# Optimization experiments

Measured on AMD Instinct MI355X. Metric: run time of the kernel, lower is better.

Reference implementation:

```python
import jax, jax.numpy as jnp
import numpy as np
from jax import lax

# ---- config (mirrors TrinityGuidance init kwargs) ----
GAMMA = 10.0        # LSE smoothing
M = 64              # RUDY grid size
THRESH = 1.0        # congestion threshold
SIGMA = 1.5         # gaussian smoothing sigma
K_SOFT = 2.0        # soft-bbox sigmoid sharpness
W_WL, W_CONG = 1.0, 0.5

B, V, P, NN, MP = 4, 20000, 400000, 50000, 32

# 4 rotation matrices (0/90/180/270 deg)
R_ALL = jnp.array([[[1, 0], [0, 1]],
                   [[0, -1], [1, 0]],
                   [[-1, 0], [0, -1]],
                   [[0, 1], [-1, 0]]], dtype=jnp.float32)


def _gauss_kernel(sigma):
    ksize = max(int(4 * sigma) | 1, 3)
    x = jnp.arange(ksize, dtype=jnp.float32) - ksize // 2
    g = jnp.exp(-x ** 2 / (2.0 * sigma ** 2))
    g2 = g[None, :] * g[:, None]
    return g2 / g2.sum()  # (k,k)


def setup_inputs() -> dict:
    key = jax.random.key(0)
    ks = jax.random.split(key, 7)
    positions = jax.random.uniform(ks[0], (B, V, 2), minval=-1.0, maxval=1.0)
    pin_to_macro = jax.random.randint(ks[1], (P,), 0, V)
    pin_offsets = jax.random.normal(ks[2], (P, 2)) * 0.01
    n2p = jax.random.randint(ks[3], (NN, MP), 0, P)
    # ragged nets: first cnt pins valid, rest padded with -1 (cnt in [2, MP])
    cnt = jax.random.randint(ks[4], (NN, 1), 2, MP + 1)
    net_to_pin = jnp.where(jnp.arange(MP)[None, :] < cnt, n2p, -1)
    rot_idx = jax.random.randint(ks[5], (B, V), 0, 4)
    rotation_onehot = jax.nn.one_hot(rot_idx, 4, dtype=jnp.float32)
    net_weights = jax.random.uniform(ks[6], (NN,), minval=0.5, maxval=1.5)
    return dict(positions=positions, net_to_pin=net_to_pin,
                pin_to_macro=pin_to_macro, pin_offsets=pin_offsets,
                rotation_onehot=rotation_onehot, net_weights=net_weights)


def _forward(positions, pin_offsets, rotation_onehot, net_weights,
             net_to_pin, pin_to_macro):
    # --- pin positions with rotated offsets ---
    macro_pos = positions[:, pin_to_macro, :]            # (B,P,2) gather
    macro_rot = rotation_onehot[:, pin_to_macro, :]      # (B,P,4)
    Rm = jnp.einsum('bpk,kij->bpij', macro_rot, R_ALL)   # (B,P,2,2)
    rotated = jnp.einsum('bpij,pj->bpi', Rm, pin_offsets)
    pin_pos = macro_pos + rotated                        # (B,P,2)

    valid = net_to_pin >= 0                              # (NN,MP)
    safe = jnp.maximum(net_to_pin, 0)
    net_pin_pos = pin_pos[:, safe, :]                    # (B,NN,MP,2)
    maskf = valid[None, :, :, None]
    masked_max = jnp.where(maskf, net_pin_pos, -1e9)
    masked_min = jnp.where(maskf, net_pin_pos, 1e9)

    # --- WA wirelength via masked double logsumexp per net ---
    gamma = jnp.float32(GAMMA)
    lse_max = jax.nn.logsumexp(gamma * masked_max, axis=2) / gamma   # (B,NN,2)
    lse_min = -jax.nn.logsumexp(-gamma * masked_min, axis=2) / gamma
    wl_per_net = (lse_max - lse_min).sum(-1)             # (B,NN)
    hpwl = (wl_per_net * net_weights[None, :]).sum(1)    # (B,)

    # --- RUDY congestion (separable soft-bbox, no (B,N,M,M) materialization) ---
    bbox_max = masked_max.max(axis=2)                    # (B,NN,2)
    bbox_min = masked_min.min(axis=2)
    bmax = (bbox_max + 1.0) * 0.5 * (M - 1)
    bmin = (bbox_min + 1.0) * 0.5 * (M - 1)
    x_min, y_min = bmin[..., 0:1], bmin[..., 1:2]        # (B,NN,1)
    x_max, y_max = bmax[..., 0:1], bmax[..., 1:2]
    g = jnp.arange(M, dtype=jnp.float32)[None, None, :]  # (1,1,M)
    in_x = jax.nn.sigmoid(K_SOFT * (g - x_min + 0.5)) * \
           jax.nn.sigmoid(K_SOFT * (x_max - g + 0.5))    # (B,NN,M)
    in_y = jax.nn.sigmoid(K_SOFT * (g - y_min + 0.5)) * \
           jax.nn.sigmoid(K_SOFT * (y_max - g + 0.5))    # (B,NN,M)
    bbox_size = jnp.maximum((x_max - x_min + 1.0) * (y_max - y_min + 1.0), 1.0)
    # rudy[b,i,j] = sum_n in_y[b,n,i] * in_x[b,n,j] / bbox_size[b,n]
    rudy = jnp.einsum('bni,bnj->bij', in_y / bbox_size, in_x)
    rudy = rudy[:, None, :, :]                           # (B,1,M,M)

    kernel = _gauss_kernel(SIGMA)                        # (k,k)
    pad = kernel.shape[-1] // 2
    rudy_smooth = lax.conv_general_dilated(
        rudy, kernel[None, None, :, :],
        window_strides=(1, 1), padding=[(pad, pad), (pad, pad)],
        dimension_numbers=('NCHW', 'OIHW', 'NCHW'))
    overflow = jax.nn.relu(rudy_smooth - THRESH)
    penalty = (overflow ** 2).sum(axis=(1, 2, 3))        # (B,)

    return W_WL * hpwl + W_CONG * penalty                # (B,)


def reference(positions, net_to_pin, pin_to_macro, pin_offsets,
              rotation_onehot, net_weights):
    return _forward(positions, pin_offsets, rotation_onehot, net_weights,
                    net_to_pin, pin_to_macro)
```

## Files before the change

### kernel.cpp

```cpp
#include <hip/hip_runtime.h>
#include <cstddef>

namespace {

constexpr int B = 4, V = 20000, P = 400000, NN = 50000, MP = 32;
constexpr float GAMMA = 10.0f, INV_GAMMA = 0.1f;
constexpr float KSOFT = 2.0f;
constexpr float THRESH = 1.0f;
constexpr float W_WL = 1.0f, W_CONG = 0.5f;
constexpr int BPB = 128;
constexpr int NET_GRID = BPB * B;
constexpr int GRPS = 7;
constexpr int NPW = GRPS * 16;
constexpr int A_SUBS = 196;
constexpr int A_GRID = A_SUBS * B;
constexpr int PREP_N = NN * MP;

typedef __attribute__((ext_vector_type(8)))  short bf16x8;
typedef __attribute__((ext_vector_type(16))) float f32x16;

__device__ __forceinline__ float fast_rcp(float x) { return __builtin_amdgcn_rcpf(x); }
__device__ __forceinline__ short f2bf(float f) {
    unsigned u = __float_as_uint(f);
    u += 0x7fffu + ((u >> 16) & 1u);
    return (short)(u >> 16);
}
template <int CTRL>
__device__ __forceinline__ float dpp_mov(float x, float id) {
    return __int_as_float(__builtin_amdgcn_update_dpp(
        __float_as_int(id), __float_as_int(x), CTRL, 0xf, 0xf, false));
}
__device__ __forceinline__ float rdlane(float x, int l) {
    return __int_as_float(__builtin_amdgcn_readlane(__float_as_int(x), l));
}
#define DPP5(x, OP, ID)                              \
    x = OP(x, dpp_mov<0x111>(x, ID));                \
    x = OP(x, dpp_mov<0x112>(x, ID));                \
    x = OP(x, dpp_mov<0x114>(x, ID));                \
    x = OP(x, dpp_mov<0x118>(x, ID));                \
    x = OP(x, dpp_mov<0x142>(x, ID));
__device__ __forceinline__ float op_add(float a, float b) { return a + b; }

__global__ void __launch_bounds__(256)
prep_kernel(const float* __restrict__ positions,
            const float* __restrict__ rot_onehot,
            float4* __restrict__ mac,
            const int* __restrict__ n2p,
            int* __restrict__ n2pT,
            float* __restrict__ zacc) {
    int i = blockIdx.x * blockDim.x + threadIdx.x;
    if (i < 2 * B) zacc[i] = 0.0f;
    if (i < B * V) {
        float2 pos = ((const float2*)positions)[i];
        float4 w = ((const float4*)rot_onehot)[i];
        mac[i] = make_float4(pos.x, pos.y, w.x - w.z, w.y - w.w);
    }
    if (i < PREP_N) {
        int n = i >> 5, j = i & 31;
        n2pT[j * NN + n] = n2p[i];
    }
}

__global__ void __launch_bounds__(256)
pin_pos_kernel(const float4* __restrict__ mac,
               const int* __restrict__ pin_to_macro,
               const float* __restrict__ pin_offsets,
               float* __restrict__ pin_pos) {
    int idx = blockIdx.x * blockDim.x + threadIdx.x;
    if (idx >= B * P / 2) return;
    int b = idx / (P / 2);
    int t = idx - b * (P / 2);
    int2 m2 = ((const int2*)pin_to_macro)[t];
    float4 o2 = ((const float4*)pin_offsets)[t];
    float4 md0 = mac[(size_t)b * V + m2.x];
    float4 md1 = mac[(size_t)b * V + m2.y];
    float4 r;
    r.x = md0.x + md0.z * o2.x - md0.w * o2.y;
    r.y = md0.y + md0.w * o2.x + md0.z * o2.y;
    r.z = md1.x + md1.z * o2.z - md1.w * o2.w;
    r.w = md1.y + md1.w * o2.z + md1.z * o2.w;
    ((float4*)pin_pos)[idx] = r;
}

__global__ void __launch_bounds__(256)
bbox_kernel(const float* __restrict__ pin_pos,
            const int* __restrict__ n2pT,
            const float* __restrict__ net_weights,
            float4* __restrict__ bbox,
            float* __restrict__ hpwl) {
    __shared__ float hps[4];
    int blk = blockIdx.x;
    int xcd = blk & 7;
    int b = xcd >> 1;
    int sub = ((blk >> 3) << 1) | (xcd & 1);
    int tid = threadIdx.x;
    int wave = tid >> 6;
    int lane = tid & 63;

    int n = sub * 256 + wave * 64 + lane;
    bool inrange = n < NN;
    int nc = inrange ? n : (NN - 1);

    const float2* pp = (const float2*)(pin_pos + (size_t)b * P * 2);

    int pi[MP];
    #pragma unroll
    for (int j = 0; j < MP; ++j) pi[j] = n2pT[j * NN + nc];

    float2 q[MP];
    #pragma unroll
    for (int j = 0; j < MP; ++j) q[j] = pp[pi[j] >= 0 ? pi[j] : 0];

    float ex1 = 0.f, ex2 = 0.f, ey1 = 0.f, ey2 = 0.f;
    float vxmax = -1e30f, vxmin = 1e30f, vymax = -1e30f, vymin = 1e30f;
    #pragma unroll
    for (int j = 0; j < MP; ++j) {
        bool v = pi[j] >= 0;
        float e1x = __expf(GAMMA * q[j].x);
        float e1y = __expf(GAMMA * q[j].y);
        ex1 += v ? e1x : 0.f;
        ex2 += v ? fast_rcp(e1x) : 0.f;
        ey1 += v ? e1y : 0.f;
        ey2 += v ? fast_rcp(e1y) : 0.f;
        vxmax = fmaxf(vxmax, v ? q[j].x : -1e30f);
        vxmin = fminf(vxmin, v ? q[j].x :  1e30f);
        vymax = fmaxf(vymax, v ? q[j].y : -1e30f);
        vymin = fminf(vymin, v ? q[j].y :  1e30f);
    }
    float w = net_weights[nc];
    float wl = __logf(ex1 * ex2 * ey1 * ey2) * INV_GAMMA;
    float hp = inrange ? wl * w : 0.f;

    if (inrange) {
        bbox[(size_t)b * NN + n] = make_float4(
            (vxmin + 1.0f) * 31.5f, (vxmax + 1.0f) * 31.5f,
            (vymin + 1.0f) * 31.5f, (vymax + 1.0f) * 31.5f);
    }
    DPP5(hp, op_add, 0.0f);
    float tot = rdlane(hp, 31) + rdlane(hp, 63);
    if (lane == 0) hps[wave] = tot;
    __syncthreads();
    if (tid == 0) atomicAdd(&hpwl[b], hps[0] + hps[1] + hps[2] + hps[3]);
}

__global__ void __launch_bounds__(256)
rudy_kernel(const float4* __restrict__ bbox,
            float* __restrict__ slabs) {
    __shared__ float lds4[4][4096];
    int x = blockIdx.x;
    int xcd = x & 7;
    int b = xcd >> 1;
    int sub = ((x >> 3) << 1) | (xcd & 1);
    int tid = threadIdx.x;
    int wave = tid >> 6;
    int lane = tid & 63;

    int s = sub * 4 + wave;
    int s0 = s * NPW;
    const float* bbf = (const float*)(bbox + (size_t)b * NN);

    #pragma unroll
    for (int k = 0; k < 7; ++k) {
        int d = s0 * 4 + k * 64 + lane;
        lds4[wave][k * 64 + lane] = bbf[d < NN * 4 ? d : 0];
    }
    const float4* st = (const float4*)lds4[wave];

    f32x16 acc00, acc01, acc10, acc11;
    #pragma unroll
    for (int r = 0; r < 16; ++r) { acc00[r] = 0.f; acc01[r] = 0.f; acc10[r] = 0.f; acc11[r] = 0.f; }

    int half8 = (lane >> 5) * 8;
    float g2 = (float)(lane & 31);

    float En0 = __expf(fmaf(-KSOFT, g2,  32.0f * KSOFT));
    float Ep0 = __expf(fmaf( KSOFT, g2, -32.0f * KSOFT));
    float EnH = __expf(-KSOFT * g2);
    float EpH = __expf( KSOFT * g2);

    if (s0 < NN) {
        float4 bbc[8];
        #pragma unroll
        for (int j = 0; j < 8; ++j) bbc[j] = st[half8 + j];
        #pragma unroll
        for (int grp = 0; grp < GRPS; ++grp) {
            float4 bbn[8];
            if (grp + 1 < GRPS) {
                #pragma unroll
                for (int j = 0; j < 8; ++j) bbn[j] = st[(grp + 1) * 16 + half8 + j];
            }
            int nb = s0 + grp * 16 + half8;
            bf16x8 A0, A1, B0, B1;
            #pragma unroll
            for (int j = 0; j < 8; ++j) {
                float4 q = bbc[j];
                float u_x = __expf(fmaf( KSOFT, q.x, -32.5f * KSOFT));
                float w_x = __expf(fmaf(-KSOFT, q.y,  31.5f * KSOFT));
                float u_y = __expf(fmaf( KSOFT, q.z, -32.5f * KSOFT));
                float w_y = __expf(fmaf(-KSOFT, q.w,  31.5f * KSOFT));
                float cx = fmaf(u_x, w_x, 1.0f);
                float cy = fmaf(u_y, w_y, 1.0f);
                float inv = (nb + j < NN)
                    ? fast_rcp(fmaxf((q.y - q.x + 1.0f) * (q.w - q.z + 1.0f), 1.0f))
                    : 0.0f;
                float a0 = fast_rcp(fmaf(En0, u_y, fmaf(Ep0, w_y, cy))) * inv;
                float a1 = fast_rcp(fmaf(EnH, u_y, fmaf(EpH, w_y, cy))) * inv;
                float b0 = fast_rcp(fmaf(En0, u_x, fmaf(Ep0, w_x, cx)));
                float b1 = fast_rcp(fmaf(EnH, u_x, fmaf(EpH, w_x, cx)));
                A0[j] = f2bf(a0); A1[j] = f2bf(a1);
                B0[j] = f2bf(b0); B1[j] = f2bf(b1);
            }
            acc00 = __builtin_amdgcn_mfma_f32_32x32x16_bf16(A0, B0, acc00, 0, 0, 0);
            acc01 = __builtin_amdgcn_mfma_f32_32x32x16_bf16(A0, B1, acc01, 0, 0, 0);
            acc10 = __builtin_amdgcn_mfma_f32_32x32x16_bf16(A1, B0, acc10, 0, 0, 0);
            acc11 = __builtin_amdgcn_mfma_f32_32x32x16_bf16(A1, B1, acc11, 0, 0, 0);
            if (grp + 1 < GRPS) {
                #pragma unroll
                for (int j = 0; j < 8; ++j) bbc[j] = bbn[j];
            }
        }
    }

    int col = lane & 31, rq = lane >> 5;
    float* wt = lds4[wave];
    #pragma unroll
    for (int r = 0; r < 16; ++r) {
        int row = (r & 3) + 8 * (r >> 2) + 4 * rq;
        wt[row * 64 + col]             = acc00[r];
        wt[row * 64 + col + 32]        = acc01[r];
        wt[(row + 32) * 64 + col]      = acc10[r];
        wt[(row + 32) * 64 + col + 32] = acc11[r];
    }
    __syncthreads();
    float* slab = slabs + ((size_t)b * BPB + sub) * 4096;
    for (int k = tid; k < 4096; k += 256)
        slab[k] = (lds4[0][k] + lds4[1][k]) + (lds4[2][k] + lds4[3][k]);
}

__global__ void __launch_bounds__(256)
rudy_reduce_kernel(const float* __restrict__ slabs, float* __restrict__ rudy) {
    int blk = blockIdx.x;
    int xcd = blk & 7;
    int b = xcd >> 1;
    int sub = ((blk >> 3) << 1) | (xcd & 1);
    int c = sub * 256 + threadIdx.x;
    const float* base = slabs + (size_t)b * BPB * 4096 + c;
    float a0 = 0.f, a1 = 0.f, a2 = 0.f, a3 = 0.f;
    #pragma unroll 4
    for (int s = 0; s < BPB; s += 4) {
        a0 += base[(size_t)(s + 0) * 4096];
        a1 += base[(size_t)(s + 1) * 4096];
        a2 += base[(size_t)(s + 2) * 4096];
        a3 += base[(size_t)(s + 3) * 4096];
    }
    rudy[b * 4096 + c] = (a0 + a1) + (a2 + a3);
}

__global__ void conv_penalty_kernel(const float* __restrict__ rudy,
                                    float* __restrict__ pen) {
    int blk = blockIdx.x;
    int b = blk >> 4, chunk = blk & 15;
    int r0 = chunk * 4;
    __shared__ float t2[10][64];
    int tid = threadIdx.x;
    for (int k = tid; k < 640; k += 256) {
        int r = k >> 6, c = k & 63, row = r0 - 3 + r;
        t2[r][c] = (row >= 0 && row < 64) ? rudy[b * 4096 + row * 64 + c] : 0.f;
    }
    __syncthreads();
    float g1[7];
    #pragma unroll
    for (int i = 0; i < 7; ++i) { float t = (float)(i - 3); g1[i] = __expf(-t * t / 4.5f); }
    float s1 = g1[0] + g1[1] + g1[2] + g1[3] + g1[4] + g1[5] + g1[6];
    float inv = fast_rcp(s1 * s1);
    int i = tid >> 6, j = tid & 63;
    float acc = 0.f;
    #pragma unroll
    for (int di = -3; di <= 3; ++di) {
        #pragma unroll
        for (int dj = -3; dj <= 3; ++dj) {
            int jj = j + dj;
            float val = (jj >= 0 && jj < 64) ? t2[i + 3 + di][jj] : 0.f;
            acc += g1[di + 3] * g1[dj + 3] * val;
        }
    }
    acc *= inv;
    float ov = acc - THRESH;
    float p = ov > 0.f ? ov * ov : 0.f;
    DPP5(p, op_add, 0.0f);
    float tot = rdlane(p, 31) + rdlane(p, 63);
    if ((tid & 63) == 0) atomicAdd(&pen[b], tot);
}

__global__ void finalize_kernel(const float* __restrict__ hpwl,
                                const float* __restrict__ pen,
                                float* __restrict__ out) {
    int i = threadIdx.x;
    if (i < B) out[i] = W_WL * hpwl[i] + W_CONG * pen[i];
}

}

extern "C" void kernel_launch(void* const* d_in, const int* in_sizes, int n_in,
                              void* d_out, int out_size, void* d_ws, size_t ws_size,
                              hipStream_t stream) {
    const float* positions    = (const float*)d_in[0];
    const int*   net_to_pin   = (const int*)d_in[1];
    const int*   pin_to_macro = (const int*)d_in[2];
    const float* pin_offsets  = (const float*)d_in[3];
    const float* rot_onehot   = (const float*)d_in[4];
    const float* net_weights  = (const float*)d_in[5];
    float* out = (float*)d_out;

    float*  pin_pos = (float*)d_ws;
    float*  rudy    = pin_pos + (size_t)B * P * 2;
    float*  hpwl    = rudy + (size_t)B * 64 * 64;
    float*  pen     = hpwl + B;
    float4* mac     = (float4*)(pen + B);
    float4* bboxb   = mac + (size_t)B * V;
    int*    n2pT    = (int*)(bboxb + (size_t)B * NN);
    float*  slabs   = pin_pos;

    prep_kernel<<<(PREP_N + 255) / 256, 256, 0, stream>>>(
        positions, rot_onehot, mac, net_to_pin, n2pT, hpwl);
    pin_pos_kernel<<<(B * P / 2 + 255) / 256, 256, 0, stream>>>(
        mac, pin_to_macro, pin_offsets, pin_pos);
    bbox_kernel<<<A_GRID, 256, 0, stream>>>(pin_pos, n2pT, net_weights, bboxb, hpwl);
    rudy_kernel<<<NET_GRID, 256, 0, stream>>>(bboxb, slabs);
    rudy_reduce_kernel<<<64, 256, 0, stream>>>(slabs, rudy);
    conv_penalty_kernel<<<64, 256, 0, stream>>>(rudy, pen);
    finalize_kernel<<<1, 64, 0, stream>>>(hpwl, pen, out);
}
```

Before: 158.3 us.

## Precompute per-net sigmoid factors once per lane and shrink RUDY LDS tiles

Each lane now computes the four exponentials and the bbox-size factor for one net once and stores them in LDS. Previously the 32 lanes sharing a net column each recomputed them inside the MFMA loop, so the inner loop is reduced to FMAs and reciprocals. Folding the bbox size into the denominator removes a multiply. The per-wave 64x64 output tiles become two shared tiles filled with LDS atomics, which cuts LDS use. The grid grows to 196 blocks per batch with 64 nets per wave, and the slabs move to a separate workspace region, adding LDS atomic contention and larger reduce input in exchange.

```diff
diff --git a/kernel.cpp b/kernel.cpp
--- a/kernel.cpp
+++ b/kernel.cpp
@@ -8,10 +8,10 @@
 constexpr float KSOFT = 2.0f;
 constexpr float THRESH = 1.0f;
 constexpr float W_WL = 1.0f, W_CONG = 0.5f;
-constexpr int BPB = 128;
+constexpr int BPB = 196;
 constexpr int NET_GRID = BPB * B;
-constexpr int GRPS = 7;
-constexpr int NPW = GRPS * 16;
+constexpr int NPW = 64;
+constexpr int GRPS = 4;
 constexpr int A_SUBS = 196;
 constexpr int A_GRID = A_SUBS * B;
 constexpr int PREP_N = NN * MP;
@@ -146,7 +146,9 @@
 __global__ void __launch_bounds__(256)
 rudy_kernel(const float4* __restrict__ bbox,
             float* __restrict__ slabs) {
-    __shared__ float lds4[4][4096];
+    __shared__ float tiles[2][4096];
+    __shared__ float4 facB[4][64];
+    __shared__ float4 facA[4][64];
     int x = blockIdx.x;
     int xcd = x & 7;
     int b = xcd >> 1;
@@ -155,16 +157,27 @@
     int wave = tid >> 6;
     int lane = tid & 63;
 
+    #pragma unroll
+    for (int k = 0; k < 32; ++k) ((float*)tiles)[k * 256 + tid] = 0.0f;
+
     int s = sub * 4 + wave;
     int s0 = s * NPW;
-    const float* bbf = (const float*)(bbox + (size_t)b * NN);
-
-    #pragma unroll
-    for (int k = 0; k < 7; ++k) {
-        int d = s0 * 4 + k * 64 + lane;
-        lds4[wave][k * 64 + lane] = bbf[d < NN * 4 ? d : 0];
-    }
-    const float4* st = (const float4*)lds4[wave];
+    const float4* bb_b = bbox + (size_t)b * NN;
+
+    {
+        int n = s0 + lane;
+        bool v = n < NN;
+        float4 q = bb_b[v ? n : 0];
+        float sz = fmaxf((q.y - q.x + 1.0f) * (q.w - q.z + 1.0f), 1.0f);
+        float ux = __expf(fmaf( KSOFT, q.x, -32.5f * KSOFT));
+        float wx = __expf(fmaf(-KSOFT, q.y,  31.5f * KSOFT));
+        float uy = __expf(fmaf( KSOFT, q.z, -32.5f * KSOFT));
+        float wy = __expf(fmaf(-KSOFT, q.w,  31.5f * KSOFT));
+        float cx = v ? fmaf(ux, wx, 1.0f)      : 3.0e38f;
+        float cy = v ? fmaf(uy, wy, 1.0f) * sz : 3.0e38f;
+        facB[wave][lane] = make_float4(ux, wx, cx, 0.f);
+        facA[wave][lane] = make_float4(uy * sz, wy * sz, cy, 0.f);
+    }
 
     f32x16 acc00, acc01, acc10, acc11;
     #pragma unroll
@@ -179,34 +192,18 @@
     float EpH = __expf( KSOFT * g2);
 
     if (s0 < NN) {
-        float4 bbc[8];
         #pragma unroll
-        for (int j = 0; j < 8; ++j) bbc[j] = st[half8 + j];
-        #pragma unroll
-        for (int grp = 0; grp < GRPS; ++grp) {
-            float4 bbn[8];
-            if (grp + 1 < GRPS) {
-                #pragma unroll
-                for (int j = 0; j < 8; ++j) bbn[j] = st[(grp + 1) * 16 + half8 + j];
-            }
-            int nb = s0 + grp * 16 + half8;
+        for (int g = 0; g < GRPS; ++g) {
             bf16x8 A0, A1, B0, B1;
             #pragma unroll
             for (int j = 0; j < 8; ++j) {
-                float4 q = bbc[j];
-                float u_x = __expf(fmaf( KSOFT, q.x, -32.5f * KSOFT));
-                float w_x = __expf(fmaf(-KSOFT, q.y,  31.5f * KSOFT));
-                float u_y = __expf(fmaf( KSOFT, q.z, -32.5f * KSOFT));
-                float w_y = __expf(fmaf(-KSOFT, q.w,  31.5f * KSOFT));
-                float cx = fmaf(u_x, w_x, 1.0f);
-                float cy = fmaf(u_y, w_y, 1.0f);
-                float inv = (nb + j < NN)
-                    ? fast_rcp(fmaxf((q.y - q.x + 1.0f) * (q.w - q.z + 1.0f), 1.0f))
-                    : 0.0f;
-                float a0 = fast_rcp(fmaf(En0, u_y, fmaf(Ep0, w_y, cy))) * inv;
-                float a1 = fast_rcp(fmaf(EnH, u_y, fmaf(EpH, w_y, cy))) * inv;
-                float b0 = fast_rcp(fmaf(En0, u_x, fmaf(Ep0, w_x, cx)));
-                float b1 = fast_rcp(fmaf(EnH, u_x, fmaf(EpH, w_x, cx)));
+                int nidx = g * 16 + half8 + j;
+                float4 fb = facB[wave][nidx];
+                float4 fa = facA[wave][nidx];
+                float b0 = fast_rcp(fmaf(En0, fb.x, fmaf(Ep0, fb.y, fb.z)));
+                float b1 = fast_rcp(fmaf(EnH, fb.x, fmaf(EpH, fb.y, fb.z)));
+                float a0 = fast_rcp(fmaf(En0, fa.x, fmaf(Ep0, fa.y, fa.z)));
+                float a1 = fast_rcp(fmaf(EnH, fa.x, fmaf(EpH, fa.y, fa.z)));
                 A0[j] = f2bf(a0); A1[j] = f2bf(a1);
                 B0[j] = f2bf(b0); B1[j] = f2bf(b1);
             }
@@ -214,27 +211,24 @@
             acc01 = __builtin_amdgcn_mfma_f32_32x32x16_bf16(A0, B1, acc01, 0, 0, 0);
             acc10 = __builtin_amdgcn_mfma_f32_32x32x16_bf16(A1, B0, acc10, 0, 0, 0);
             acc11 = __builtin_amdgcn_mfma_f32_32x32x16_bf16(A1, B1, acc11, 0, 0, 0);
-            if (grp + 1 < GRPS) {
-                #pragma unroll
-                for (int j = 0; j < 8; ++j) bbc[j] = bbn[j];
-            }
         }
     }
 
+    __syncthreads();
     int col = lane & 31, rq = lane >> 5;
-    float* wt = lds4[wave];
+    float* wt = tiles[wave >> 1];
     #pragma unroll
     for (int r = 0; r < 16; ++r) {
         int row = (r & 3) + 8 * (r >> 2) + 4 * rq;
-        wt[row * 64 + col]             = acc00[r];
-        wt[row * 64 + col + 32]        = acc01[r];
-        wt[(row + 32) * 64 + col]      = acc10[r];
-        wt[(row + 32) * 64 + col + 32] = acc11[r];
+        atomicAdd(&wt[row * 64 + col],             acc00[r]);
+        atomicAdd(&wt[row * 64 + col + 32],        acc01[r]);
+        atomicAdd(&wt[(row + 32) * 64 + col],      acc10[r]);
+        atomicAdd(&wt[(row + 32) * 64 + col + 32], acc11[r]);
     }
     __syncthreads();
     float* slab = slabs + ((size_t)b * BPB + sub) * 4096;
     for (int k = tid; k < 4096; k += 256)
-        slab[k] = (lds4[0][k] + lds4[1][k]) + (lds4[2][k] + lds4[3][k]);
+        slab[k] = tiles[0][k] + tiles[1][k];
 }
 
 __global__ void __launch_bounds__(256)
@@ -319,7 +313,7 @@
     float4* mac     = (float4*)(pen + B);
     float4* bboxb   = mac + (size_t)B * V;
     int*    n2pT    = (int*)(bboxb + (size_t)B * NN);
-    float*  slabs   = pin_pos;
+    float*  slabs   = (float*)(n2pT + (size_t)NN * MP);
 
     prep_kernel<<<(PREP_N + 255) / 256, 256, 0, stream>>>(
         positions, rot_onehot, mac, net_to_pin, n2pT, hpwl);
```

Result: slower. 227.0 us (+43.4%).
